# Optimization experiments

Measured on AMD Instinct MI355X. Metric: run time of the kernel, lower is better.

Reference implementation:

```python
import jax, jax.numpy as jnp
import numpy as np

B, D, H = 65536, 3, 256  # collocation batch, coord dim, hidden width


def setup_inputs() -> dict:
    key = jax.random.key(0)
    ks = jax.random.split(key, 8)

    def init(k, shape, fan_in):
        return jax.random.normal(k, shape, dtype=jnp.float32) * np.float32(1.0 / np.sqrt(fan_in))

    return {
        "x": jax.random.uniform(ks[0], (B, D), dtype=jnp.float32, minval=0.1, maxval=1.0),
        "W0": init(ks[1], (D, H), D), "b0": jnp.zeros((H,), jnp.float32),
        "W1": init(ks[2], (H, H), H), "b1": jnp.zeros((H,), jnp.float32),
        "W2": init(ks[3], (H, H), H), "b2": jnp.zeros((H,), jnp.float32),
        "W3": init(ks[4], (H, H), H), "b3": jnp.zeros((H,), jnp.float32),
        "Wout": init(ks[5], (H, 1), H), "bout": jnp.zeros((1,), jnp.float32),
    }


def reference(x, W0, b0, W1, b1, W2, b2, W3, b3, Wout, bout):
    # Scalar PINN network u(xi), xi: [D]
    def u_fn(xi):
        h = jnp.tanh(xi @ W0 + b0)
        h = jnp.tanh(h @ W1 + b1)
        h = jnp.tanh(h @ W2 + b2)
        h = jnp.tanh(h @ W3 + b3)
        return (h @ Wout + bout)[0]

    u = jax.vmap(u_fn)(x)                               # [B]
    # batch_gradient: du/dx_i for every coordinate axis (Cartesian: no adjustment)
    grads = jax.vmap(jax.grad(u_fn))(x)                 # [B, D]
    # batch_hessian diagonal: d^2u/dx_i^2 via forward-over-reverse
    hess_fn = jax.jacfwd(jax.grad(u_fn))                # [D, D] per sample
    hess_diag = jax.vmap(lambda xi: jnp.diagonal(hess_fn(xi)))(x)  # [B, D]
    # pack (u, grad, hessian-diagonal) as the PDE-residual ingredients
    return jnp.concatenate([u[:, None], grads, hess_diag], axis=1)  # [B, 1+D+D]
```

## Files before the change

kernel.cpp:

```cpp
#include <hip/hip_runtime.h>
#include <hip/hip_fp16.h>

#define HDIM 256
#define MS 16
#define LDAK 264

typedef _Float16 half8 __attribute__((ext_vector_type(8)));
typedef _Float16 half4 __attribute__((ext_vector_type(4)));
typedef _Float16 half2v __attribute__((ext_vector_type(2)));
typedef float f32x4 __attribute__((ext_vector_type(4)));

__device__ __forceinline__ float fast_tanh(float x) {
    float e = __expf(2.0f * x);
    return 1.0f - 2.0f * __builtin_amdgcn_rcpf(e + 1.0f);
}

__device__ __forceinline__ half4 cvt4(float a, float b, float c, float d) {
    half2v lo = __builtin_bit_cast(half2v, __builtin_amdgcn_cvt_pkrtz(a, b));
    half2v hi = __builtin_bit_cast(half2v, __builtin_amdgcn_cvt_pkrtz(c, d));
    half4 r; r[0] = lo[0]; r[1] = lo[1]; r[2] = hi[0]; r[3] = hi[1];
    return r;
}

__global__ __launch_bounds__(256) void pack_weights(const float* __restrict__ W1,
                                                    const float* __restrict__ W2,
                                                    const float* __restrict__ W3,
                                                    _Float16* __restrict__ out) {
    int tid = blockIdx.x * 256 + threadIdx.x;
    int l = tid >> 13;
    int idx = tid & 8191;
    int kg = idx >> 8;
    int n = idx & 255;
    const float* W = (l == 0) ? W1 : (l == 1) ? W2 : W3;
    half8 v;
    #pragma unroll
    for (int j = 0; j < 8; ++j) v[j] = (_Float16)W[(kg * 8 + j) * 256 + n];
    *(half8*)(out + l * 65536 + (kg * 256 + n) * 8) = v;
}

__global__ __launch_bounds__(256, 2)
void pinn_fused(const float* __restrict__ x,
                const float* __restrict__ W0,
                const float* __restrict__ b0,
                const float* __restrict__ b1,
                const float* __restrict__ b2,
                const float* __restrict__ b3,
                const float* __restrict__ Wout,
                const float* __restrict__ bout,
                const _Float16* __restrict__ Wp,
                float* __restrict__ out) {
    __shared__ __align__(16) _Float16 Abuf[7 * MS][LDAK];
    __shared__ float xs[MS * 3];

    const int tid  = threadIdx.x;
    const int lane = tid & 63;
    const int wid  = tid >> 6;
    const int qd   = lane >> 4;
    const int n15  = lane & 15;
    const int base = blockIdx.x * MS;
    const int nw   = wid * 64 + n15;

    if (tid < MS * 3) xs[tid] = x[base * 3 + tid];

    half8 wf[3][4];
    #pragma unroll
    for (int t = 0; t < 4; ++t)
        wf[0][t] = *(const half8*)(Wp + ((0 * 4 + qd) * 256 + nw + t * 16) * 8);
    #pragma unroll
    for (int t = 0; t < 4; ++t)
        wf[1][t] = *(const half8*)(Wp + ((1 * 4 + qd) * 256 + nw + t * 16) * 8);

    __syncthreads();

    {
        const int m  = tid & 15;
        const int nb = (tid >> 4) * 16;
        const float x0 = xs[m * 3 + 0], x1 = xs[m * 3 + 1], x2 = xs[m * 3 + 2];
        #pragma unroll
        for (int ch = 0; ch < 2; ++ch) {
            const int n0 = nb + ch * 8;
            half8 h[7];
            #pragma unroll
            for (int r = 0; r < 8; ++r) {
                const int n = n0 + r;
                const float w0 = W0[n], w1 = W0[HDIM + n], w2 = W0[2 * HDIM + n];
                float z  = x0 * w0 + x1 * w1 + x2 * w2 + b0[n];
                float tv = fast_tanh(z);
                float dd = 1.f - tv * tv;
                float c2 = -2.f * tv * dd;
                h[0][r] = (_Float16)tv;
                h[1][r] = (_Float16)(dd * w0);
                h[2][r] = (_Float16)(dd * w1);
                h[3][r] = (_Float16)(dd * w2);
                h[4][r] = (_Float16)(c2 * w0 * w0);
                h[5][r] = (_Float16)(c2 * w1 * w1);
                h[6][r] = (_Float16)(c2 * w2 * w2);
            }
            #pragma unroll
            for (int c = 0; c < 7; ++c)
                *(half8*)&Abuf[c * MS + m][n0] = h[c];
        }
    }
    __syncthreads();

    #pragma unroll
    for (int l = 0; l < 3; ++l) {
        const float* bb = (l == 0) ? b1 : (l == 1) ? b2 : b3;

        f32x4 acc[7][4];
        #pragma unroll
        for (int c = 0; c < 7; ++c)
            #pragma unroll
            for (int t = 0; t < 4; ++t) acc[c][t] = (f32x4){0.f, 0.f, 0.f, 0.f};

        #pragma unroll
        for (int s = 0; s < 8; ++s) {
            const int g = l * 8 + s;
            if (g + 2 < 24) {
                const _Float16* Wn = Wp + ((g + 2) >> 3) * 65536;
                const int sn = (g + 2) & 7;
                #pragma unroll
                for (int t = 0; t < 4; ++t)
                    wf[(g + 2) % 3][t] =
                        *(const half8*)(Wn + ((sn * 4 + qd) * 256 + nw + t * 16) * 8);
            }
            half8 af[7];
            #pragma unroll
            for (int c = 0; c < 7; ++c)
                af[c] = *(const half8*)&Abuf[c * MS + n15][s * 32 + qd * 8];
            #pragma unroll
            for (int c = 0; c < 7; ++c)
                #pragma unroll
                for (int t = 0; t < 4; ++t)
                    acc[c][t] = __builtin_amdgcn_mfma_f32_16x16x32_f16(wf[g % 3][t], af[c], acc[c][t], 0, 0, 0);
        }
        __syncthreads();

        #pragma unroll
        for (int t = 0; t < 4; ++t) {
            const int ncol = wid * 64 + t * 16 + qd * 4;
            f32x4 bv = *(const f32x4*)(bb + ncol);
            float tv[4], gj[3][4], sj[3][4];
            #pragma unroll
            for (int r = 0; r < 4; ++r) {
                float zv = acc[0][t][r] + bv[r];
                tv[r] = fast_tanh(zv);
                float dd = 1.f - tv[r] * tv[r];
                float c2 = -2.f * tv[r] * dd;
                #pragma unroll
                for (int i = 0; i < 3; ++i) {
                    float zg = acc[1 + i][t][r];
                    float zs = acc[4 + i][t][r];
                    gj[i][r] = dd * zg;
                    sj[i][r] = dd * zs + c2 * zg * zg;
                }
            }
            *(half4*)&Abuf[0 * MS + n15][ncol] = cvt4(tv[0], tv[1], tv[2], tv[3]);
            #pragma unroll
            for (int i = 0; i < 3; ++i) {
                *(half4*)&Abuf[(1 + i) * MS + n15][ncol] = cvt4(gj[i][0], gj[i][1], gj[i][2], gj[i][3]);
                *(half4*)&Abuf[(4 + i) * MS + n15][ncol] = cvt4(sj[i][0], sj[i][1], sj[i][2], sj[i][3]);
            }
        }
        __syncthreads();
    }

    if (tid < 7 * MS * 2) {
        const int row = tid >> 1;
        const int h   = tid & 1;
        const _Float16* rp = &Abuf[row][h * 128];
        const float* wp = Wout + h * 128;
        float accv = 0.f;
        #pragma unroll 4
        for (int k = 0; k < 128; k += 8) {
            half8 av = *(const half8*)&rp[k];
            #pragma unroll
            for (int j = 0; j < 8; ++j) accv += (float)av[j] * wp[k + j];
        }
        accv += __shfl_xor(accv, 1, 64);
        if (h == 0) {
            const int c = row >> 4;
            const int m = row & 15;
            if (c == 0) accv += bout[0];
            out[(base + m) * 7 + c] = accv;
        }
    }
}

extern "C" void kernel_launch(void* const* d_in, const int* in_sizes, int n_in,
                              void* d_out, int out_size, void* d_ws, size_t ws_size,
                              hipStream_t stream) {
    const float* xp   = (const float*)d_in[0];
    const float* W0   = (const float*)d_in[1];
    const float* b0   = (const float*)d_in[2];
    const float* W1   = (const float*)d_in[3];
    const float* b1   = (const float*)d_in[4];
    const float* W2   = (const float*)d_in[5];
    const float* b2   = (const float*)d_in[6];
    const float* W3   = (const float*)d_in[7];
    const float* b3   = (const float*)d_in[8];
    const float* Wout = (const float*)d_in[9];
    const float* bout = (const float*)d_in[10];
    _Float16* Wp = (_Float16*)d_ws;

    pack_weights<<<96, 256, 0, stream>>>(W1, W2, W3, Wp);
    pinn_fused<<<65536 / MS, 256, 0, stream>>>(xp, W0, b0, b1, b2, b3, Wout, bout, Wp,
                                               (float*)d_out);
}
```

Baseline: 255.3 us.

## Halve samples per block and pack seven derivative channels into four MFMA tiles

Cuts samples per block from 16 to 8 and lays out the 7 propagated channels (value, 3 gradients, 3 Hessian diagonals) as 56 rows padded to 64. That fits them into 4 MFMA row tiles instead of 7. Partner channels in the same tile are exchanged with DPP row-xor-8 swaps, so each lane can apply the chain rule for its own channel. The accumulator and weight-prefetch register footprint shrinks (triple-buffered weights become double-buffered), so launch bounds target 3 blocks per CU for better latency hiding. In exchange, each sample does slightly more MFMA work because of the padding row. Twice as many blocks each stream the full weight set, which doubles weight traffic from L2.

```diff
diff --git a/kernel.cpp b/kernel.cpp
--- a/kernel.cpp
+++ b/kernel.cpp
@@ -2,7 +2,7 @@
 #include <hip/hip_fp16.h>
 
 #define HDIM 256
-#define MS 16
+#define MS 8
 #define LDAK 264
 
 typedef _Float16 half8 __attribute__((ext_vector_type(8)));
@@ -20,6 +20,12 @@
     half2v hi = __builtin_bit_cast(half2v, __builtin_amdgcn_cvt_pkrtz(c, d));
     half4 r; r[0] = lo[0]; r[1] = lo[1]; r[2] = hi[0]; r[3] = hi[1];
     return r;
+}
+
+__device__ __forceinline__ float dpp_xor8(float v) {
+    int r = __builtin_amdgcn_update_dpp(0, __builtin_bit_cast(int, v),
+                                        0x128, 0xf, 0xf, true);
+    return __builtin_bit_cast(float, r);
 }
 
 __global__ __launch_bounds__(256) void pack_weights(const float* __restrict__ W1,
@@ -38,7 +44,7 @@
     *(half8*)(out + l * 65536 + (kg * 256 + n) * 8) = v;
 }
 
-__global__ __launch_bounds__(256, 2)
+__global__ __launch_bounds__(256, 3)
 void pinn_fused(const float* __restrict__ x,
                 const float* __restrict__ W0,
                 const float* __restrict__ b0,
@@ -49,7 +55,7 @@
                 const float* __restrict__ bout,
                 const _Float16* __restrict__ Wp,
                 float* __restrict__ out) {
-    __shared__ __align__(16) _Float16 Abuf[7 * MS][LDAK];
+    __shared__ __align__(16) _Float16 Abuf[8 * MS][LDAK];
     __shared__ float xs[MS * 3];
 
     const int tid  = threadIdx.x;
@@ -57,49 +63,44 @@
     const int wid  = tid >> 6;
     const int qd   = lane >> 4;
     const int n15  = lane & 15;
+    const bool ev  = (lane & 8) == 0;
     const int base = blockIdx.x * MS;
     const int nw   = wid * 64 + n15;
 
     if (tid < MS * 3) xs[tid] = x[base * 3 + tid];
 
-    half8 wf[3][4];
+    half8 wf[2][4];
     #pragma unroll
     for (int t = 0; t < 4; ++t)
         wf[0][t] = *(const half8*)(Wp + ((0 * 4 + qd) * 256 + nw + t * 16) * 8);
-    #pragma unroll
-    for (int t = 0; t < 4; ++t)
-        wf[1][t] = *(const half8*)(Wp + ((1 * 4 + qd) * 256 + nw + t * 16) * 8);
 
     __syncthreads();
 
     {
-        const int m  = tid & 15;
-        const int nb = (tid >> 4) * 16;
+        const int m  = tid >> 5;
+        const int n0 = (tid & 31) * 8;
         const float x0 = xs[m * 3 + 0], x1 = xs[m * 3 + 1], x2 = xs[m * 3 + 2];
-        #pragma unroll
-        for (int ch = 0; ch < 2; ++ch) {
-            const int n0 = nb + ch * 8;
-            half8 h[7];
-            #pragma unroll
-            for (int r = 0; r < 8; ++r) {
-                const int n = n0 + r;
-                const float w0 = W0[n], w1 = W0[HDIM + n], w2 = W0[2 * HDIM + n];
-                float z  = x0 * w0 + x1 * w1 + x2 * w2 + b0[n];
-                float tv = fast_tanh(z);
-                float dd = 1.f - tv * tv;
-                float c2 = -2.f * tv * dd;
-                h[0][r] = (_Float16)tv;
-                h[1][r] = (_Float16)(dd * w0);
-                h[2][r] = (_Float16)(dd * w1);
-                h[3][r] = (_Float16)(dd * w2);
-                h[4][r] = (_Float16)(c2 * w0 * w0);
-                h[5][r] = (_Float16)(c2 * w1 * w1);
-                h[6][r] = (_Float16)(c2 * w2 * w2);
-            }
-            #pragma unroll
-            for (int c = 0; c < 7; ++c)
-                *(half8*)&Abuf[c * MS + m][n0] = h[c];
-        }
+        half8 h[7];
+        #pragma unroll
+        for (int r = 0; r < 8; ++r) {
+            const int n = n0 + r;
+            const float w0 = W0[n], w1 = W0[HDIM + n], w2 = W0[2 * HDIM + n];
+            float z  = x0 * w0 + x1 * w1 + x2 * w2 + b0[n];
+            float tv = fast_tanh(z);
+            float dd = 1.f - tv * tv;
+            float c2 = -2.f * tv * dd;
+            h[0][r] = (_Float16)tv;
+            h[1][r] = (_Float16)(dd * w0);
+            h[2][r] = (_Float16)(dd * w1);
+            h[3][r] = (_Float16)(dd * w2);
+            h[4][r] = (_Float16)(c2 * w0 * w0);
+            h[5][r] = (_Float16)(c2 * w1 * w1);
+            h[6][r] = (_Float16)(c2 * w2 * w2);
+        }
+        #pragma unroll
+        for (int c = 0; c < 7; ++c)
+            *(half8*)&Abuf[c * 8 + m][n0] = h[c];
+        *(half8*)&Abuf[56 + m][n0] = (half8)(_Float16)0.f;
     }
     __syncthreads();
 
@@ -107,32 +108,32 @@
     for (int l = 0; l < 3; ++l) {
         const float* bb = (l == 0) ? b1 : (l == 1) ? b2 : b3;
 
-        f32x4 acc[7][4];
-        #pragma unroll
-        for (int c = 0; c < 7; ++c)
-            #pragma unroll
-            for (int t = 0; t < 4; ++t) acc[c][t] = (f32x4){0.f, 0.f, 0.f, 0.f};
+        f32x4 acc[4][4];
+        #pragma unroll
+        for (int T = 0; T < 4; ++T)
+            #pragma unroll
+            for (int t = 0; t < 4; ++t) acc[T][t] = (f32x4){0.f, 0.f, 0.f, 0.f};
 
         #pragma unroll
         for (int s = 0; s < 8; ++s) {
             const int g = l * 8 + s;
-            if (g + 2 < 24) {
-                const _Float16* Wn = Wp + ((g + 2) >> 3) * 65536;
-                const int sn = (g + 2) & 7;
+            if (g + 1 < 24) {
+                const _Float16* Wn = Wp + ((g + 1) >> 3) * 65536;
+                const int sn = (g + 1) & 7;
                 #pragma unroll
                 for (int t = 0; t < 4; ++t)
-                    wf[(g + 2) % 3][t] =
+                    wf[(g + 1) & 1][t] =
                         *(const half8*)(Wn + ((sn * 4 + qd) * 256 + nw + t * 16) * 8);
             }
-            half8 af[7];
-            #pragma unroll
-            for (int c = 0; c < 7; ++c)
-                af[c] = *(const half8*)&Abuf[c * MS + n15][s * 32 + qd * 8];
-            #pragma unroll
-            for (int c = 0; c < 7; ++c)
+            half8 af[4];
+            #pragma unroll
+            for (int T = 0; T < 4; ++T)
+                af[T] = *(const half8*)&Abuf[T * 16 + n15][s * 32 + qd * 8];
+            #pragma unroll
+            for (int T = 0; T < 4; ++T)
                 #pragma unroll
                 for (int t = 0; t < 4; ++t)
-                    acc[c][t] = __builtin_amdgcn_mfma_f32_16x16x32_f16(wf[g % 3][t], af[c], acc[c][t], 0, 0, 0);
+                    acc[T][t] = __builtin_amdgcn_mfma_f32_16x16x32_f16(wf[g & 1][t], af[T], acc[T][t], 0, 0, 0);
         }
         __syncthreads();
 
@@ -140,47 +141,53 @@
         for (int t = 0; t < 4; ++t) {
             const int ncol = wid * 64 + t * 16 + qd * 4;
             f32x4 bv = *(const f32x4*)(bb + ncol);
-            float tv[4], gj[3][4], sj[3][4];
+            float o0[4], o1[4], o2[4], o3[4];
             #pragma unroll
             for (int r = 0; r < 4; ++r) {
-                float zv = acc[0][t][r] + bv[r];
-                tv[r] = fast_tanh(zv);
-                float dd = 1.f - tv[r] * tv[r];
-                float c2 = -2.f * tv[r] * dd;
-                #pragma unroll
-                for (int i = 0; i < 3; ++i) {
-                    float zg = acc[1 + i][t][r];
-                    float zs = acc[4 + i][t][r];
-                    gj[i][r] = dd * zg;
-                    sj[i][r] = dd * zs + c2 * zg * zg;
-                }
+                float a0 = acc[0][t][r], a1 = acc[1][t][r];
+                float a2 = acc[2][t][r], a3 = acc[3][t][r];
+                float zv = a0 + (ev ? bv[r] : 0.f);
+                float tv = fast_tanh(zv);
+                float dd = 1.f - tv * tv;
+                float c2 = -2.f * tv * dd;
+                float P0 = dpp_xor8(a0);
+                float P1 = dpp_xor8(a1);
+                float Pd = dpp_xor8(dd);
+                float Pc = dpp_xor8(c2);
+                float dU = ev ? dd : Pd;
+                float cU = ev ? c2 : Pc;
+                float zgA = ev ? P0 : P1;
+                o0[r] = ev ? tv : dU * a0;
+                o1[r] = dU * a1;
+                o2[r] = dU * a2 + cU * zgA * zgA;
+                o3[r] = ev ? (dU * a3 + cU * P1 * P1)
+                           : 0.f;
             }
-            *(half4*)&Abuf[0 * MS + n15][ncol] = cvt4(tv[0], tv[1], tv[2], tv[3]);
-            #pragma unroll
-            for (int i = 0; i < 3; ++i) {
-                *(half4*)&Abuf[(1 + i) * MS + n15][ncol] = cvt4(gj[i][0], gj[i][1], gj[i][2], gj[i][3]);
-                *(half4*)&Abuf[(4 + i) * MS + n15][ncol] = cvt4(sj[i][0], sj[i][1], sj[i][2], sj[i][3]);
-            }
+            *(half4*)&Abuf[0 * 16 + n15][ncol] = cvt4(o0[0], o0[1], o0[2], o0[3]);
+            *(half4*)&Abuf[1 * 16 + n15][ncol] = cvt4(o1[0], o1[1], o1[2], o1[3]);
+            *(half4*)&Abuf[2 * 16 + n15][ncol] = cvt4(o2[0], o2[1], o2[2], o2[3]);
+            *(half4*)&Abuf[3 * 16 + n15][ncol] = cvt4(o3[0], o3[1], o3[2], o3[3]);
         }
         __syncthreads();
     }
 
-    if (tid < 7 * MS * 2) {
-        const int row = tid >> 1;
-        const int h   = tid & 1;
-        const _Float16* rp = &Abuf[row][h * 128];
-        const float* wp = Wout + h * 128;
+    if (tid < 56 * 4) {
+        const int row = tid >> 2;
+        const int q   = tid & 3;
+        const _Float16* rp = &Abuf[row][q * 64];
+        const float* wp = Wout + q * 64;
         float accv = 0.f;
-        #pragma unroll 4
-        for (int k = 0; k < 128; k += 8) {
-            half8 av = *(const half8*)&rp[k];
-            #pragma unroll
-            for (int j = 0; j < 8; ++j) accv += (float)av[j] * wp[k + j];
+        #pragma unroll
+        for (int kg = 0; kg < 8; ++kg) {
+            half8 av = *(const half8*)&rp[kg * 8];
+            #pragma unroll
+            for (int j = 0; j < 8; ++j) accv += (float)av[j] * wp[kg * 8 + j];
         }
         accv += __shfl_xor(accv, 1, 64);
-        if (h == 0) {
-            const int c = row >> 4;
-            const int m = row & 15;
+        accv += __shfl_xor(accv, 2, 64);
+        if (q == 0) {
+            const int c = row >> 3;
+            const int m = row & 7;
             if (c == 0) accv += bout[0];
             out[(base + m) * 7 + c] = accv;
         }
```

Result: slower. 315.2 us (+23.5%).

## Ping-pong two half-blocks offset by one stage to overlap MFMA and tanh phases

Applied to the files above, without the earlier changes.

Blocks become 512 threads, each holding two independent 16-sample halves with separate shared buffers. The halves run the same stage sequence offset by one step, so while one does an MFMA layer the other does the elementwise tanh/derivative phase. This is meant to overlap matrix-core and VALU work inside a CU. It also adds software prefetch of A fragments within each K stage and reloads weights per layer rather than across layers. The costs are more barriers per block (9 iterations), doubled LDS per block, and possible occupancy changes with launch_bounds(512,2).

```diff
diff --git a/kernel.cpp b/kernel.cpp
--- a/kernel.cpp
+++ b/kernel.cpp
@@ -4,6 +4,8 @@
 #define HDIM 256
 #define MS 16
 #define LDAK 264
+#define ABUF_HALVES (7 * MS * LDAK)
+#define SMEM_BYTES (2 * ABUF_HALVES * 2)
 
 typedef _Float16 half8 __attribute__((ext_vector_type(8)));
 typedef _Float16 half4 __attribute__((ext_vector_type(4)));
@@ -38,7 +40,7 @@
     *(half8*)(out + l * 65536 + (kg * 256 + n) * 8) = v;
 }
 
-__global__ __launch_bounds__(256, 2)
+__global__ __launch_bounds__(512, 2)
 void pinn_fused(const float* __restrict__ x,
                 const float* __restrict__ W0,
                 const float* __restrict__ b0,
@@ -49,33 +51,28 @@
                 const float* __restrict__ bout,
                 const _Float16* __restrict__ Wp,
                 float* __restrict__ out) {
-    __shared__ __align__(16) _Float16 Abuf[7 * MS][LDAK];
-    __shared__ float xs[MS * 3];
+    extern __shared__ __align__(16) _Float16 smem[];
 
     const int tid  = threadIdx.x;
     const int lane = tid & 63;
     const int wid  = tid >> 6;
+    const int hf   = wid >> 2;
+    const int wid4 = wid & 3;
     const int qd   = lane >> 4;
     const int n15  = lane & 15;
-    const int base = blockIdx.x * MS;
-    const int nw   = wid * 64 + n15;
-
-    if (tid < MS * 3) xs[tid] = x[base * 3 + tid];
-
-    half8 wf[3][4];
-    #pragma unroll
-    for (int t = 0; t < 4; ++t)
-        wf[0][t] = *(const half8*)(Wp + ((0 * 4 + qd) * 256 + nw + t * 16) * 8);
-    #pragma unroll
-    for (int t = 0; t < 4; ++t)
-        wf[1][t] = *(const half8*)(Wp + ((1 * 4 + qd) * 256 + nw + t * 16) * 8);
-
-    __syncthreads();
-
-    {
-        const int m  = tid & 15;
-        const int nb = (tid >> 4) * 16;
-        const float x0 = xs[m * 3 + 0], x1 = xs[m * 3 + 1], x2 = xs[m * 3 + 2];
+    const int ht   = tid & 255;
+    _Float16* Abuf = smem + hf * ABUF_HALVES;
+    const int base = blockIdx.x * 32 + hf * MS;
+    const int nw   = wid4 * 64 + n15;
+
+    f32x4 acc[7][4];
+
+    auto stage_init = [&]() {
+        const int m  = ht & 15;
+        const int nb = (ht >> 4) * 16;
+        const float x0 = x[(base + m) * 3 + 0];
+        const float x1 = x[(base + m) * 3 + 1];
+        const float x2 = x[(base + m) * 3 + 2];
         #pragma unroll
         for (int ch = 0; ch < 2; ++ch) {
             const int n0 = nb + ch * 8;
@@ -98,47 +95,52 @@
             }
             #pragma unroll
             for (int c = 0; c < 7; ++c)
-                *(half8*)&Abuf[c * MS + m][n0] = h[c];
-        }
-    }
-    __syncthreads();
-
-    #pragma unroll
-    for (int l = 0; l < 3; ++l) {
-        const float* bb = (l == 0) ? b1 : (l == 1) ? b2 : b3;
-
-        f32x4 acc[7][4];
+                *(half8*)&Abuf[(c * MS + m) * LDAK + n0] = h[c];
+        }
+    };
+
+    auto stage_k = [&](const _Float16* W) {
         #pragma unroll
         for (int c = 0; c < 7; ++c)
             #pragma unroll
             for (int t = 0; t < 4; ++t) acc[c][t] = (f32x4){0.f, 0.f, 0.f, 0.f};
-
+        half8 wf[3][4];
+        #pragma unroll
+        for (int t = 0; t < 4; ++t)
+            wf[0][t] = *(const half8*)(W + ((0 * 4 + qd) * 256 + nw + t * 16) * 8);
+        #pragma unroll
+        for (int t = 0; t < 4; ++t)
+            wf[1][t] = *(const half8*)(W + ((1 * 4 + qd) * 256 + nw + t * 16) * 8);
+        half8 af[2][7];
+        #pragma unroll
+        for (int c = 0; c < 7; ++c)
+            af[0][c] = *(const half8*)&Abuf[(c * MS + n15) * LDAK + qd * 8];
         #pragma unroll
         for (int s = 0; s < 8; ++s) {
-            const int g = l * 8 + s;
-            if (g + 2 < 24) {
-                const _Float16* Wn = Wp + ((g + 2) >> 3) * 65536;
-                const int sn = (g + 2) & 7;
+            if (s < 6) {
                 #pragma unroll
                 for (int t = 0; t < 4; ++t)
-                    wf[(g + 2) % 3][t] =
-                        *(const half8*)(Wn + ((sn * 4 + qd) * 256 + nw + t * 16) * 8);
-            }
-            half8 af[7];
+                    wf[(s + 2) % 3][t] =
+                        *(const half8*)(W + (((s + 2) * 4 + qd) * 256 + nw + t * 16) * 8);
+            }
+            if (s < 7) {
+                #pragma unroll
+                for (int c = 0; c < 7; ++c)
+                    af[(s + 1) & 1][c] =
+                        *(const half8*)&Abuf[(c * MS + n15) * LDAK + (s + 1) * 32 + qd * 8];
+            }
             #pragma unroll
             for (int c = 0; c < 7; ++c)
-                af[c] = *(const half8*)&Abuf[c * MS + n15][s * 32 + qd * 8];
-            #pragma unroll
-            for (int c = 0; c < 7; ++c)
                 #pragma unroll
                 for (int t = 0; t < 4; ++t)
-                    acc[c][t] = __builtin_amdgcn_mfma_f32_16x16x32_f16(wf[g % 3][t], af[c], acc[c][t], 0, 0, 0);
-        }
-        __syncthreads();
-
+                    acc[c][t] = __builtin_amdgcn_mfma_f32_16x16x32_f16(wf[s % 3][t], af[s & 1][c], acc[c][t], 0, 0, 0);
+        }
+    };
+
+    auto stage_elem = [&](const float* bb) {
         #pragma unroll
         for (int t = 0; t < 4; ++t) {
-            const int ncol = wid * 64 + t * 16 + qd * 4;
+            const int ncol = wid4 * 64 + t * 16 + qd * 4;
             f32x4 bv = *(const f32x4*)(bb + ncol);
             float tv[4], gj[3][4], sj[3][4];
             #pragma unroll
@@ -155,35 +157,53 @@
                     sj[i][r] = dd * zs + c2 * zg * zg;
                 }
             }
-            *(half4*)&Abuf[0 * MS + n15][ncol] = cvt4(tv[0], tv[1], tv[2], tv[3]);
+            *(half4*)&Abuf[(0 * MS + n15) * LDAK + ncol] = cvt4(tv[0], tv[1], tv[2], tv[3]);
             #pragma unroll
             for (int i = 0; i < 3; ++i) {
-                *(half4*)&Abuf[(1 + i) * MS + n15][ncol] = cvt4(gj[i][0], gj[i][1], gj[i][2], gj[i][3]);
-                *(half4*)&Abuf[(4 + i) * MS + n15][ncol] = cvt4(sj[i][0], sj[i][1], sj[i][2], sj[i][3]);
-            }
+                *(half4*)&Abuf[((1 + i) * MS + n15) * LDAK + ncol] =
+                    cvt4(gj[i][0], gj[i][1], gj[i][2], gj[i][3]);
+                *(half4*)&Abuf[((4 + i) * MS + n15) * LDAK + ncol] =
+                    cvt4(sj[i][0], sj[i][1], sj[i][2], sj[i][3]);
+            }
+        }
+    };
+
+    auto stage_out = [&]() {
+        if (ht < 7 * MS * 2) {
+            const int row = ht >> 1;
+            const int h   = ht & 1;
+            const _Float16* rp = &Abuf[row * LDAK + h * 128];
+            const float* wp = Wout + h * 128;
+            float accv = 0.f;
+            #pragma unroll 4
+            for (int k = 0; k < 128; k += 8) {
+                half8 av = *(const half8*)&rp[k];
+                #pragma unroll
+                for (int j = 0; j < 8; ++j) accv += (float)av[j] * wp[k + j];
+            }
+            accv += __shfl_xor(accv, 1, 64);
+            if (h == 0) {
+                const int c = row >> 4;
+                const int m = row & 15;
+                if (c == 0) accv += bout[0];
+                out[(base + m) * 7 + c] = accv;
+            }
+        }
+    };
+
+    #pragma unroll 1
+    for (int iv = 0; iv < 9; ++iv) {
+        const int p = iv - hf;
+        if (p == 0) {
+            stage_init();
+        } else if (p == 1 || p == 3 || p == 5) {
+            stage_k(Wp + ((p - 1) >> 1) * 65536);
+        } else if (p == 2 || p == 4 || p == 6) {
+            stage_elem(p == 2 ? b1 : (p == 4 ? b2 : b3));
+        } else if (p == 7) {
+            stage_out();
         }
         __syncthreads();
-    }
-
-    if (tid < 7 * MS * 2) {
-        const int row = tid >> 1;
-        const int h   = tid & 1;
-        const _Float16* rp = &Abuf[row][h * 128];
-        const float* wp = Wout + h * 128;
-        float accv = 0.f;
-        #pragma unroll 4
-        for (int k = 0; k < 128; k += 8) {
-            half8 av = *(const half8*)&rp[k];
-            #pragma unroll
-            for (int j = 0; j < 8; ++j) accv += (float)av[j] * wp[k + j];
-        }
-        accv += __shfl_xor(accv, 1, 64);
-        if (h == 0) {
-            const int c = row >> 4;
-            const int m = row & 15;
-            if (c == 0) accv += bout[0];
-            out[(base + m) * 7 + c] = accv;
-        }
     }
 }
 
@@ -203,7 +223,11 @@
     const float* bout = (const float*)d_in[10];
     _Float16* Wp = (_Float16*)d_ws;
 
+    hipFuncSetAttribute((const void*)pinn_fused,
+                        hipFuncAttributeMaxDynamicSharedMemorySize, SMEM_BYTES);
+
     pack_weights<<<96, 256, 0, stream>>>(W1, W2, W3, Wp);
-    pinn_fused<<<65536 / MS, 256, 0, stream>>>(xp, W0, b0, b1, b2, b3, Wout, bout, Wp,
-                                               (float*)d_out);
-}
+    pinn_fused<<<65536 / 32, 512, SMEM_BYTES, stream>>>(xp, W0, b0, b1, b2, b3,
+                                                        Wout, bout, Wp,
+                                                        (float*)d_out);
+}
```

Result: slower. 289.9 us (+13.5%).
